# Performance work log

Hardware: AMD Instinct MI355X
Metric: run time of the kernel (lower is better)

The kernel has to match this reference:

```python
import jax, jax.numpy as jnp
import numpy as np

B, S, D, H, F, R = 4, 128, 512, 8, 2048, 8
DH = D // H
THRESH = 0.1  # hardcoded in the torch module


def _ln(x, g, b):
    m = x.mean(-1, keepdims=True)
    v = ((x - m) ** 2).mean(-1, keepdims=True)
    return (x - m) * jax.lax.rsqrt(v + 1e-5) * g + b


def setup_inputs() -> dict:
    key = jax.random.key(0)
    ks = jax.random.split(key, 12)
    w = lambda k, shape, std: jax.random.normal(k, shape, jnp.float32) * std
    s = 1.0 / np.sqrt(D)
    qk_std = 2.0 / np.sqrt(D)  # peaky attention so adjacency threshold fires
    return {
        "x": jax.random.normal(ks[0], (B, S, D), jnp.float32),
        "ln1_g": jnp.ones(D, jnp.float32), "ln1_b": jnp.zeros(D, jnp.float32),
        "wq": w(ks[1], (D, D), qk_std), "bq": jnp.zeros(D, jnp.float32),
        "wk": w(ks[2], (D, D), qk_std), "bk": jnp.zeros(D, jnp.float32),
        "wv": w(ks[3], (D, D), s), "bv": jnp.zeros(D, jnp.float32),
        "wo": w(ks[4], (D, D), s), "bo": jnp.zeros(D, jnp.float32),
        "w1": w(ks[5], (D, F), s), "b1": jnp.zeros(F, jnp.float32),
        "w2": w(ks[6], (F, D), 1.0 / np.sqrt(F)), "b2": jnp.zeros(D, jnp.float32),
        "rc_w1": w(ks[7], (2 * D, D), 1.0 / np.sqrt(2 * D)), "rc_b1": jnp.zeros(D, jnp.float32),
        "rc_w2": w(ks[8], (D, R), s), "rc_b2": jnp.zeros(R, jnp.float32),
        "kg_w": w(ks[9], (R, D, D), s),
        "s2n_w": w(ks[10], (D, D), s), "s2n_b": jnp.zeros(D, jnp.float32),
        "ln2_g": jnp.ones(D, jnp.float32), "ln2_b": jnp.zeros(D, jnp.float32),
    }


def reference(x, ln1_g, ln1_b, wq, bq, wk, bk, wv, bv, wo, bo,
              w1, b1, w2, b2, rc_w1, rc_b1, rc_w2, rc_b2,
              kg_w, s2n_w, s2n_b, ln2_g, ln2_b):
    # pre-norm attention
    xn = _ln(x, ln1_g, ln1_b)
    q = (xn @ wq + bq).reshape(B, S, H, DH)
    k = (xn @ wk + bk).reshape(B, S, H, DH)
    v = (xn @ wv + bv).reshape(B, S, H, DH)
    scores = jnp.einsum('bihd,bjhd->bhij', q, k) / np.sqrt(DH)
    attn = jax.nn.softmax(scores, axis=-1)                  # [B,H,S,S]
    ctx = jnp.einsum('bhij,bjhd->bihd', attn, v).reshape(B, S, D)
    attn_out = ctx @ wo + bo
    # FFN -> neural_understanding (no residual, as in source)
    nu = jax.nn.relu(attn_out @ w1 + b1) @ w2 + b2          # [B,S,D]
    # dynamic edge extraction, expressed as a dense mask (jit-safe)
    am = attn.mean(axis=1)                                  # [B,S,S]
    adj = (am > THRESH) & (~jnp.eye(S, dtype=bool))         # u != v
    # relation classifier on every (u,v) pair; mask selects real edges
    a_part = nu @ rc_w1[:D]                                 # concept1 half
    b_part = nu @ rc_w1[D:]                                 # concept2 half
    h = jax.nn.relu(a_part[:, :, None, :] + b_part[:, None, :, :] + rc_b1)  # [B,S,S,D]
    logits = h @ rc_w2 + rc_b2                              # [B,S,S,R]
    pred = jnp.argmax(logits, axis=-1)
    valid = adj & (pred != 0)                               # relation 0 == NONE
    oh = jax.nn.one_hot(pred, R, dtype=nu.dtype) * valid[..., None].astype(nu.dtype)
    # RGCN-style knowledge graph conv: message u -> v with per-relation weight
    transformed = jnp.einsum('bud,rde->bure', nu, kg_w)     # [B,S,R,D]
    agg = jnp.einsum('buvr,bure->bve', oh, transformed)     # [B,S,D]
    reasoned = nu + agg
    neural_result = reasoned @ s2n_w + s2n_b
    out = _ln(x + neural_result, ln2_g, ln2_b)
    return out
```

## Files before the change

### kernel.cpp

```cpp
#include <hip/hip_runtime.h>
#include <hip/hip_bf16.h>

#define B_ 4
#define S_ 128
#define D_ 512
#define H_ 8
#define DH_ 64
#define F_ 2048
#define R_ 8
#define BS_ (B_ * S_)
#define BSD_ (BS_ * D_)
#define E_ 262144

typedef __attribute__((ext_vector_type(8))) short short8;
typedef __attribute__((ext_vector_type(4))) float f32x4;
typedef __attribute__((ext_vector_type(4))) unsigned short ushort4v;

__device__ __forceinline__ void split2(float a, unsigned short& h, unsigned short& l) {
    unsigned u = __float_as_uint(a);
    unsigned hr = (u + 0x7FFFu + ((u >> 16) & 1u)) >> 16;
    h = (unsigned short)hr;
    float lo = a - __uint_as_float(hr << 16);
    unsigned u2 = __float_as_uint(lo);
    l = (unsigned short)((u2 + 0x7FFFu + ((u2 >> 16) & 1u)) >> 16);
}

struct TDesc { const float* s; unsigned short* h; unsigned short* l; int K; int N; int off; };
struct TPack { TDesc d[10]; };

__global__ void prep_kernel(TPack p, int nt, const float* __restrict__ x,
                            const float* __restrict__ g, const float* __restrict__ be,
                            unsigned short* __restrict__ xh, unsigned short* __restrict__ xl) {
    __shared__ float tr[32][33];
    __shared__ float red[256];
    int bid = blockIdx.x;
    if (bid < nt) {
        int wi = 0;
#pragma unroll
        for (int i = 1; i < 10; ++i) if (bid >= p.d[i].off) wi = i;
        const TDesc dd = p.d[wi];
        int t = bid - dd.off;
        int ntk = dd.K / 32;
        int tk = t % ntk, tn = t / ntk;
        int k0 = tk * 32, n0 = tn * 32;
        int col = threadIdx.x & 31, rg = threadIdx.x >> 5;
#pragma unroll
        for (int i = 0; i < 4; ++i) {
            int row = rg * 4 + i;
            tr[row][col] = dd.s[(size_t)(k0 + row) * dd.N + n0 + col];
        }
        __syncthreads();
#pragma unroll
        for (int i = 0; i < 4; ++i) {
            int n = n0 + rg * 4 + i;
            int k = k0 + col;
            unsigned short h, l;
            split2(tr[col][rg * 4 + i], h, l);
            dd.h[(size_t)n * dd.K + k] = h;
            dd.l[(size_t)n * dd.K + k] = l;
        }
    } else {
        int row = bid - nt;
        int t = threadIdx.x;
        const float* xr = x + (size_t)row * D_;
        float v0 = xr[t], v1 = xr[t + 256];
        red[t] = v0 + v1;
        __syncthreads();
        for (int off = 128; off > 0; off >>= 1) { if (t < off) red[t] += red[t + off]; __syncthreads(); }
        float mean = red[0] * (1.0f / D_);
        __syncthreads();
        float d0 = v0 - mean, d1 = v1 - mean;
        red[t] = d0 * d0 + d1 * d1;
        __syncthreads();
        for (int off = 128; off > 0; off >>= 1) { if (t < off) red[t] += red[t + off]; __syncthreads(); }
        float rs = rsqrtf(red[0] * (1.0f / D_) + 1e-5f);
        float o0 = d0 * rs * g[t] + be[t];
        float o1 = d1 * rs * g[t + 256] + be[t + 256];
        unsigned short h, l;
        split2(o0, h, l); xh[(size_t)row * D_ + t] = h;       xl[(size_t)row * D_ + t] = l;
        split2(o1, h, l); xh[(size_t)row * D_ + t + 256] = h; xl[(size_t)row * D_ + t + 256] = l;
    }
}

struct GemmLds {
    unsigned short A[2][2][64][64];
    unsigned short B[2][2][64][64];
};

__device__ __forceinline__ void gload16(const unsigned short* g, unsigned short* l) {
    __builtin_amdgcn_global_load_lds(
        (const __attribute__((address_space(1))) void*)g,
        (__attribute__((address_space(3))) void*)l, 16, 0, 0);
}

__device__ __forceinline__ void mgemm_core(const unsigned short* __restrict__ Ath,
                                           const unsigned short* __restrict__ Atl,
                                           const unsigned short* __restrict__ Bth,
                                           const unsigned short* __restrict__ Btl,
                                           int K, int rowBase, int colBase,
                                           int kStart, int nsteps,
                                           f32x4 acc[2][2], GemmLds* L) {
    int tid = threadIdx.x;
    int w = tid >> 6, lane = tid & 63;
    int lm = lane & 15, quad = lane >> 4;
    int wm = (w & 1) * 32, wn = (w >> 1) * 32;
    int r0 = w * 8 + (lane >> 3);
    int lc = ((lane & 7) ^ (lane >> 3)) * 8;
    int wb = w * 512;
    size_t a0 = (size_t)(rowBase + r0) * K + kStart + lc;
    size_t a1 = (size_t)(rowBase + r0 + 32) * K + kStart + lc;
    size_t b0 = (size_t)(colBase + r0) * K + kStart + lc;
    size_t b1 = (size_t)(colBase + r0 + 32) * K + kStart + lc;
    unsigned short* AB = &L->A[0][0][0][0];
    unsigned short* BB = &L->B[0][0][0][0];
    auto stage = [&](int p, size_t koff) {
        gload16(&Ath[a0 + koff], AB + p * 8192 + wb);
        gload16(&Ath[a1 + koff], AB + p * 8192 + 2048 + wb);
        gload16(&Atl[a0 + koff], AB + p * 8192 + 4096 + wb);
        gload16(&Atl[a1 + koff], AB + p * 8192 + 6144 + wb);
        gload16(&Bth[b0 + koff], BB + p * 8192 + wb);
        gload16(&Bth[b1 + koff], BB + p * 8192 + 2048 + wb);
        gload16(&Btl[b0 + koff], BB + p * 8192 + 4096 + wb);
        gload16(&Btl[b1 + koff], BB + p * 8192 + 6144 + wb);
    };
    stage(0, 0);
    __syncthreads();
    for (int s = 0; s < nsteps; ++s) {
        int p = s & 1;
        if (s + 1 < nsteps) stage(p ^ 1, (size_t)(s + 1) * 64);
#pragma unroll
        for (int sub = 0; sub < 2; ++sub) {
            short8 ah[2], al[2], bh[2], bl[2];
            int pc = ((sub * 4 + quad) ^ (lm & 7)) * 8;
#pragma unroll
            for (int t = 0; t < 2; ++t) {
                int ra = (wm + t * 16 + lm) * 64 + pc;
                int rb = (wn + t * 16 + lm) * 64 + pc;
                ah[t] = *(const short8*)(AB + p * 8192 + ra);
                al[t] = *(const short8*)(AB + p * 8192 + 4096 + ra);
                bh[t] = *(const short8*)(BB + p * 8192 + rb);
                bl[t] = *(const short8*)(BB + p * 8192 + 4096 + rb);
            }
#pragma unroll
            for (int tm = 0; tm < 2; ++tm)
#pragma unroll
                for (int tn = 0; tn < 2; ++tn) {
                    acc[tm][tn] = __builtin_amdgcn_mfma_f32_16x16x32_bf16(ah[tm], bh[tn], acc[tm][tn], 0, 0, 0);
                    acc[tm][tn] = __builtin_amdgcn_mfma_f32_16x16x32_bf16(ah[tm], bl[tn], acc[tm][tn], 0, 0, 0);
                    acc[tm][tn] = __builtin_amdgcn_mfma_f32_16x16x32_bf16(al[tm], bh[tn], acc[tm][tn], 0, 0, 0);
                }
        }
        __syncthreads();
    }
}

__device__ __forceinline__ void gemm_epilogue(f32x4 acc[2][2], const float* bias,
                                              float* Cf, unsigned short* Ch, unsigned short* Cl,
                                              int N, int relu, int rowBase, int colBase) {
    int tid = threadIdx.x;
    int w = tid >> 6, lane = tid & 63;
    int lm = lane & 15, quad = lane >> 4;
    int wm = (w & 1) * 32, wn = (w >> 1) * 32;
#pragma unroll
    for (int tm = 0; tm < 2; ++tm)
#pragma unroll
        for (int tn = 0; tn < 2; ++tn) {
            int col = colBase + wn + tn * 16 + lm;
            float bi = bias ? bias[col] : 0.f;
#pragma unroll
            for (int r = 0; r < 4; ++r) {
                int row = rowBase + wm + tm * 16 + quad * 4 + r;
                float v = acc[tm][tn][r] + bi;
                if (relu) v = fmaxf(v, 0.f);
                size_t o = (size_t)row * N + col;
                if (Cf) Cf[o] = v;
                if (Ch) {
                    unsigned short sh, sl;
                    split2(v, sh, sl);
                    Ch[o] = sh; Cl[o] = sl;
                }
            }
        }
}

__global__ __launch_bounds__(256) void mgemm_kernel(const unsigned short* __restrict__ Ath,
                                                    const unsigned short* __restrict__ Atl,
                                                    const unsigned short* __restrict__ Bth,
                                                    const unsigned short* __restrict__ Btl,
                                                    const float* __restrict__ bias,
                                                    float* __restrict__ Cf,
                                                    unsigned short* __restrict__ Ch,
                                                    unsigned short* __restrict__ Cl,
                                                    int N, int K, int relu) {
    __shared__ GemmLds L;
    int rowBase = blockIdx.y * 64, colBase = blockIdx.x * 64;
    f32x4 acc[2][2] = {};
    mgemm_core(Ath, Atl, Bth, Btl, K, rowBase, colBase, 0, K / 64, acc, &L);
    gemm_epilogue(acc, bias, Cf, Ch, Cl, N, relu, rowBase, colBase);
}

__global__ __launch_bounds__(256) void mgemm_zw_kernel(const unsigned short* __restrict__ Ath,
                                                       const unsigned short* __restrict__ Atl,
                                                       const unsigned short* __restrict__ Bth,
                                                       const unsigned short* __restrict__ Btl,
                                                       const float* __restrict__ b0,
                                                       const float* __restrict__ b1,
                                                       const float* __restrict__ b2,
                                                       float* __restrict__ Cbase,
                                                       int M, int N, int K) {
    __shared__ GemmLds L;
    int z = blockIdx.z;
    const unsigned short* bth = Bth + (size_t)z * K * N;
    const unsigned short* btl = Btl + (size_t)z * K * N;
    const float* bias = (z == 0) ? b0 : (z == 1) ? b1 : b2;
    float* C = Cbase + (size_t)z * M * N;
    int rowBase = blockIdx.y * 64, colBase = blockIdx.x * 64;
    f32x4 acc[2][2] = {};
    mgemm_core(Ath, Atl, bth, btl, K, rowBase, colBase, 0, K / 64, acc, &L);
    gemm_epilogue(acc, bias, C, nullptr, nullptr, N, 0, rowBase, colBase);
}

__global__ __launch_bounds__(256) void mgemm_part_kernel(const unsigned short* __restrict__ Ath,
                                                         const unsigned short* __restrict__ Atl,
                                                         const unsigned short* __restrict__ Bth,
                                                         const unsigned short* __restrict__ Btl,
                                                         float* __restrict__ Cbase,
                                                         int M, int N, int K) {
    __shared__ GemmLds L;
    int ks = gridDim.z, z = blockIdx.z;
    int kLen = K / ks, kStart = z * kLen;
    float* C = Cbase + (size_t)z * M * N;
    int rowBase = blockIdx.y * 64, colBase = blockIdx.x * 64;
    f32x4 acc[2][2] = {};
    mgemm_core(Ath, Atl, Bth, Btl, K, rowBase, colBase, kStart, kLen / 64, acc, &L);
    gemm_epilogue(acc, nullptr, C, nullptr, nullptr, N, 0, rowBase, colBase);
}

__global__ __launch_bounds__(256) void wo_adj_kernel(const unsigned short* __restrict__ Ath,
                                                     const unsigned short* __restrict__ Atl,
                                                     const unsigned short* __restrict__ Bth,
                                                     const unsigned short* __restrict__ Btl,
                                                     const float* __restrict__ bias,
                                                     unsigned short* __restrict__ Ch,
                                                     unsigned short* __restrict__ Cl,
                                                     const float* __restrict__ attnP,
                                                     unsigned long long* __restrict__ adjm) {
    __shared__ GemmLds L;
    int bid = blockIdx.x;
    if (bid < 64) {
        int rowBase = (bid >> 3) * 64, colBase = (bid & 7) * 64;
        f32x4 acc[2][2] = {};
        mgemm_core(Ath, Atl, Bth, Btl, D_, rowBase, colBase, 0, D_ / 64, acc, &L);
        gemm_epilogue(acc, bias, nullptr, Ch, Cl, D_, 0, rowBase, colBase);
    } else {
        int idx = (bid - 64) * 256 + threadIdx.x;
        int j = idx & (S_ - 1);
        int bi = idx >> 7;
        int i = bi & (S_ - 1);
        int b = bi >> 7;
        float s = 0.f;
#pragma unroll
        for (int h = 0; h < H_; ++h) s += attnP[(((size_t)(b * H_ + h)) * S_ + i) * S_ + j];
        s *= (1.0f / H_);
        int pred = (s > 0.1f && i != j) ? 1 : 0;
        unsigned long long m = __ballot(pred);
        if ((threadIdx.x & 63) == 0)
            adjm[(size_t)bi * 2 + ((threadIdx.x >> 6) & 1)] = m;
    }
}

__global__ void reduce4_kernel(const float* __restrict__ part, const float* __restrict__ b2,
                               float* __restrict__ nu,
                               unsigned short* __restrict__ nh, unsigned short* __restrict__ nl) {
    int base = blockIdx.x * 1024 + threadIdx.x * 4;
    f32x4 s = *(const f32x4*)&b2[base & (D_ - 1)];
#pragma unroll
    for (int z = 0; z < 4; ++z) s += *(const f32x4*)&part[(size_t)z * BSD_ + base];
    *(f32x4*)&nu[base] = s;
    ushort4v hv, lv;
#pragma unroll
    for (int i = 0; i < 4; ++i) { unsigned short h, l; split2(s[i], h, l); hv[i] = h; lv[i] = l; }
    *(ushort4v*)&nh[base] = hv;
    *(ushort4v*)&nl[base] = lv;
}

__global__ void reduce8_kernel(const float* __restrict__ part, const float* __restrict__ nu,
                               unsigned short* __restrict__ rh, unsigned short* __restrict__ rl) {
    int base = blockIdx.x * 1024 + threadIdx.x * 4;
    f32x4 s = *(const f32x4*)&nu[base];
#pragma unroll
    for (int z = 0; z < 8; ++z) s += *(const f32x4*)&part[(size_t)z * BSD_ + base];
    ushort4v hv, lv;
#pragma unroll
    for (int i = 0; i < 4; ++i) { unsigned short h, l; split2(s[i], h, l); hv[i] = h; lv[i] = l; }
    *(ushort4v*)&rh[base] = hv;
    *(ushort4v*)&rl[base] = lv;
}

__global__ __launch_bounds__(512) void attn_kernel2(const float* __restrict__ q,
                                                    const float* __restrict__ k,
                                                    const float* __restrict__ v,
                                                    float* __restrict__ attnP,
                                                    unsigned short* __restrict__ ch,
                                                    unsigned short* __restrict__ cl) {
    __shared__ float ksm[S_][DH_ + 3];
    __shared__ float qsm[16][DH_];
    __shared__ float psm[16][S_];
    int tid = threadIdx.x;
    int w = tid >> 6, lane = tid & 63;
    int blk = blockIdx.x;
    int ig = blk & 7;
    int bh = blk >> 3;
    int h = bh & (H_ - 1);
    int b = bh >> 3;
    int i0 = ig * 16;
    const float* kb = k + (size_t)b * S_ * D_ + h * DH_;
    for (int j = w; j < S_; j += 8) ksm[j][lane] = kb[(size_t)j * D_ + lane];
    for (int il = w; il < 16; il += 8)
        qsm[il][lane] = q[(size_t)(b * S_ + i0 + il) * D_ + h * DH_ + lane];
    __syncthreads();
    const float* vb = v + (size_t)b * S_ * D_ + h * DH_ + lane;
#pragma unroll
    for (int c = 0; c < 2; ++c) {
        int il = w + c * 8;
        int i = i0 + il;
        float s0 = 0.f, s1 = 0.f;
#pragma unroll 8
        for (int d = 0; d < DH_; ++d) {
            float qd = qsm[il][d];
            s0 += qd * ksm[lane][d];
            s1 += qd * ksm[lane + 64][d];
        }
        s0 *= 0.125f; s1 *= 0.125f;
        float m = fmaxf(s0, s1);
#pragma unroll
        for (int off = 32; off > 0; off >>= 1) m = fmaxf(m, __shfl_xor(m, off));
        float e0 = __expf(s0 - m), e1 = __expf(s1 - m);
        float sum = e0 + e1;
#pragma unroll
        for (int off = 32; off > 0; off >>= 1) sum += __shfl_xor(sum, off);
        float inv = 1.f / sum;
        float p0 = e0 * inv, p1 = e1 * inv;
        float* arow = attnP + ((size_t)(b * H_ + h) * S_ + i) * S_;
        arow[lane] = p0;
        arow[lane + 64] = p1;
        psm[il][lane] = p0;
        psm[il][lane + 64] = p1;
        float acc = 0.f;
        for (int j = 0; j < S_; ++j) acc += psm[il][j] * vb[(size_t)j * D_];
        unsigned short sh, sl;
        split2(acc, sh, sl);
        size_t o = (size_t)(b * S_ + i) * D_ + h * DH_ + lane;
        ch[o] = sh; cl[o] = sl;
    }
}

__global__ __launch_bounds__(512) void mbuild_edge_kernel(const float* __restrict__ nu,
                                                          const float* __restrict__ a_part,
                                                          const float* __restrict__ b_part,
                                                          const float* __restrict__ rc_b1,
                                                          const float* __restrict__ rc_w2,
                                                          const float* __restrict__ rc_b2,
                                                          const unsigned long long* __restrict__ adjm,
                                                          unsigned short* __restrict__ Mh,
                                                          unsigned short* __restrict__ Ml) {
    __shared__ float acc[R_ * D_];
    __shared__ float w2t[R_][D_];
    __shared__ float bsm[D_];
    __shared__ int rl[S_];
    int blk = blockIdx.x;
    int vv = blk & (S_ - 1);
    int b = blk >> 7;
    int t = threadIdx.x;
    int w = t >> 6, lane = t & 63;
    for (int i = t; i < R_ * D_; i += 512) {
        w2t[i & 7][i >> 3] = rc_w2[i];
        acc[i] = 0.f;
    }
    bsm[t] = b_part[(size_t)blk * D_ + t];
    __syncthreads();
    int wsel = vv >> 6, bsh = vv & 63;
    for (int u = w; u < S_; u += 8) {
        unsigned long long word = adjm[((size_t)(b * S_ + u)) * 2 + wsel];
        if ((word >> bsh) & 1ull) {
            const float* ap = a_part + (size_t)(b * S_ + u) * D_;
            float lp[R_];
#pragma unroll
            for (int r = 0; r < R_; ++r) lp[r] = 0.f;
#pragma unroll
            for (int jj = 0; jj < D_ / 64; ++jj) {
                int d = lane + jj * 64;
                float hv = fmaxf(ap[d] + bsm[d] + rc_b1[d], 0.f);
#pragma unroll
                for (int r = 0; r < R_; ++r) lp[r] += hv * w2t[r][d];
            }
#pragma unroll
            for (int r = 0; r < R_; ++r) {
#pragma unroll
                for (int off = 32; off > 0; off >>= 1) lp[r] += __shfl_down(lp[r], off);
            }
            if (lane == 0) {
                float best = lp[0] + rc_b2[0];
                int bi = 0;
#pragma unroll
                for (int r = 1; r < R_; ++r) {
                    float L = lp[r] + rc_b2[r];
                    if (L > best) { best = L; bi = r; }
                }
                rl[u] = bi;
            }
        } else if (lane == 0) {
            rl[u] = 0;
        }
    }
    __syncthreads();
    for (int u = 0; u < S_; ++u) {
        int r = rl[u];
        if (r > 0) acc[r * D_ + t] += nu[(size_t)(b * S_ + u) * D_ + t];
    }
    __syncthreads();
    unsigned short* Hrow = Mh + (size_t)blk * (R_ * D_);
    unsigned short* Lrow = Ml + (size_t)blk * (R_ * D_);
    for (int i = t; i < R_ * D_; i += 512) {
        unsigned short sh, sl;
        split2(acc[i], sh, sl);
        Hrow[i] = sh; Lrow[i] = sl;
    }
}

__global__ void ln2_kernel(const float* __restrict__ x, const float* __restrict__ y,
                           const float* __restrict__ g, const float* __restrict__ be,
                           float* __restrict__ out) {
    int row = blockIdx.x;
    int t = threadIdx.x;
    __shared__ float red[256];
    float v0 = x[row * D_ + t]       + y[row * D_ + t];
    float v1 = x[row * D_ + t + 256] + y[row * D_ + t + 256];
    red[t] = v0 + v1;
    __syncthreads();
    for (int off = 128; off > 0; off >>= 1) {
        if (t < off) red[t] += red[t + off];
        __syncthreads();
    }
    float mean = red[0] * (1.0f / D_);
    __syncthreads();
    float d0 = v0 - mean, d1 = v1 - mean;
    red[t] = d0 * d0 + d1 * d1;
    __syncthreads();
    for (int off = 128; off > 0; off >>= 1) {
        if (t < off) red[t] += red[t + off];
        __syncthreads();
    }
    float rs = rsqrtf(red[0] * (1.0f / D_) + 1e-5f);
    out[row * D_ + t]       = d0 * rs * g[t]       + be[t];
    out[row * D_ + t + 256] = d1 * rs * g[t + 256] + be[t + 256];
}

extern "C" void kernel_launch(void* const* d_in, const int* in_sizes, int n_in,
                              void* d_out, int out_size, void* d_ws, size_t ws_size,
                              hipStream_t stream) {
    const float* x     = (const float*)d_in[0];
    const float* ln1_g = (const float*)d_in[1];
    const float* ln1_b = (const float*)d_in[2];
    const float* wq    = (const float*)d_in[3];
    const float* bq    = (const float*)d_in[4];
    const float* wk    = (const float*)d_in[5];
    const float* bk    = (const float*)d_in[6];
    const float* wv    = (const float*)d_in[7];
    const float* bv    = (const float*)d_in[8];
    const float* wo    = (const float*)d_in[9];
    const float* bo    = (const float*)d_in[10];
    const float* w1    = (const float*)d_in[11];
    const float* b1    = (const float*)d_in[12];
    const float* w2    = (const float*)d_in[13];
    const float* b2    = (const float*)d_in[14];
    const float* rc_w1 = (const float*)d_in[15];
    const float* rc_b1 = (const float*)d_in[16];
    const float* rc_w2 = (const float*)d_in[17];
    const float* rc_b2 = (const float*)d_in[18];
    const float* kg_w  = (const float*)d_in[19];
    const float* s2n_w = (const float*)d_in[20];
    const float* s2n_b = (const float*)d_in[21];
    const float* ln2_g = (const float*)d_in[22];
    const float* ln2_b = (const float*)d_in[23];
    float* out = (float*)d_out;

    const int BS  = BS_;
    const int BSD = BSD_;

    unsigned short* wt = (unsigned short*)d_ws;
    unsigned short* qkv_h = wt;
    unsigned short* qkv_l = wt + 3 * E_;
    unsigned short* wo_h  = wt + 6 * E_;
    unsigned short* wo_l  = wt + 7 * E_;
    unsigned short* w1_h  = wt + 8 * E_;
    unsigned short* w1_l  = wt + 12 * E_;
    unsigned short* w2_h  = wt + 16 * E_;
    unsigned short* w2_l  = wt + 20 * E_;
    unsigned short* rc_h  = wt + 24 * E_;
    unsigned short* rc_l  = wt + 26 * E_;
    unsigned short* kg_h  = wt + 28 * E_;
    unsigned short* kg_l  = wt + 36 * E_;
    unsigned short* s2_h  = wt + 44 * E_;
    unsigned short* s2_l  = wt + 45 * E_;

    unsigned short* xn_h  = wt + 46 * E_;
    unsigned short* xn_l  = xn_h + BSD;
    unsigned short* ctx_h = xn_l + BSD;
    unsigned short* ctx_l = ctx_h + BSD;
    unsigned short* ao_h  = ctx_l + BSD;
    unsigned short* ao_l  = ao_h + BSD;
    unsigned short* hid_h = ao_l + BSD;
    unsigned short* hid_l = hid_h + (size_t)BS * F_;
    unsigned short* nu_h  = hid_l + (size_t)BS * F_;
    unsigned short* nu_l  = nu_h + BSD;
    unsigned short* mb_h  = nu_l + BSD;
    unsigned short* mb_l  = mb_h + (size_t)BS * R_ * D_;
    unsigned short* rs_h  = mb_l + (size_t)BS * R_ * D_;
    unsigned short* rs_l  = rs_h + BSD;

    float* fbase  = (float*)(rs_l + BSD);
    float* q      = fbase;
    float* v_     = q + 2 * BSD;
    float* apart  = q + 3 * BSD;
    float* nu     = apart + 2 * BSD;
    float* y      = nu + BSD;
    float* part4  = y + BSD;
    float* part8  = part4 + 4 * BSD;
    float* attnP  = part8 + 8 * BSD;

    unsigned long long* adjm = (unsigned long long*)(attnP + 2097152);

    TPack tp;
    int off = 0;
    auto setd = [&](int i, const float* s, unsigned short* h, unsigned short* l, int K, int N) {
        tp.d[i] = TDesc{s, h, l, K, N, off};
        off += (K / 32) * (N / 32);
    };
    setd(0, wq, qkv_h,          qkv_l,          D_, D_);
    setd(1, wk, qkv_h + E_,     qkv_l + E_,     D_, D_);
    setd(2, wv, qkv_h + 2 * E_, qkv_l + 2 * E_, D_, D_);
    setd(3, wo, wo_h, wo_l, D_, D_);
    setd(4, w1, w1_h, w1_l, D_, F_);
    setd(5, w2, w2_h, w2_l, F_, D_);
    setd(6, rc_w1,            rc_h,      rc_l,      D_, D_);
    setd(7, rc_w1 + D_ * D_,  rc_h + E_, rc_l + E_, D_, D_);
    setd(8, kg_w, kg_h, kg_l, R_ * D_, D_);
    setd(9, s2n_w, s2_h, s2_l, D_, D_);
    hipLaunchKernelGGL(prep_kernel, dim3(off + BS), dim3(256), 0, stream, tp, off,
                       x, ln1_g, ln1_b, xn_h, xn_l);

    hipLaunchKernelGGL(mgemm_zw_kernel, dim3(D_ / 64, BS / 64, 3), dim3(256), 0, stream,
                       xn_h, xn_l, qkv_h, qkv_l, bq, bk, bv, q, BS, D_, D_);
    hipLaunchKernelGGL(attn_kernel2, dim3(B_ * H_ * 8), dim3(512), 0, stream,
                       q, q + BSD, v_, attnP, ctx_h, ctx_l);
    hipLaunchKernelGGL(wo_adj_kernel, dim3(64 + 256), dim3(256), 0, stream,
                       ctx_h, ctx_l, wo_h, wo_l, bo, ao_h, ao_l, attnP, adjm);
    hipLaunchKernelGGL(mgemm_kernel, dim3(F_ / 64, BS / 64), dim3(256), 0, stream,
                       ao_h, ao_l, w1_h, w1_l, b1, (float*)nullptr, hid_h, hid_l, F_, D_, 1);
    hipLaunchKernelGGL(mgemm_part_kernel, dim3(D_ / 64, BS / 64, 4), dim3(256), 0, stream,
                       hid_h, hid_l, w2_h, w2_l, part4, BS, D_, F_);
    hipLaunchKernelGGL(reduce4_kernel, dim3(BSD / 1024), dim3(256), 0, stream,
                       part4, b2, nu, nu_h, nu_l);
    hipLaunchKernelGGL(mgemm_zw_kernel, dim3(D_ / 64, BS / 64, 2), dim3(256), 0, stream,
                       nu_h, nu_l, rc_h, rc_l, (const float*)nullptr, (const float*)nullptr,
                       (const float*)nullptr, apart, BS, D_, D_);
    hipLaunchKernelGGL(mbuild_edge_kernel, dim3(BS), dim3(512), 0, stream,
                       nu, apart, apart + BSD, rc_b1, rc_w2, rc_b2, adjm, mb_h, mb_l);
    hipLaunchKernelGGL(mgemm_part_kernel, dim3(D_ / 64, BS / 64, 8), dim3(256), 0, stream,
                       mb_h, mb_l, kg_h, kg_l, part8, BS, D_, R_ * D_);
    hipLaunchKernelGGL(reduce8_kernel, dim3(BSD / 1024), dim3(256), 0, stream,
                       part8, nu, rs_h, rs_l);
    hipLaunchKernelGGL(mgemm_kernel, dim3(D_ / 64, BS / 64), dim3(256), 0, stream,
                       rs_h, rs_l, s2_h, s2_l, s2n_b, y, (unsigned short*)nullptr,
                       (unsigned short*)nullptr, D_, D_, 0);
    hipLaunchKernelGGL(ln2_kernel, dim3(BS), dim3(256), 0, stream, x, y, ln2_g, ln2_b, out);
}
```

Measured before the change: 224.1 us.

## Triple-buffer GEMM LDS staging with explicit vmcnt waits

Moves the split-bf16 GEMM core from double to triple buffering in LDS, keeping up to two future K-steps of global-to-LDS loads in flight. Plain __syncthreads is replaced by explicit s_waitcnt vmcnt counts plus s_barrier and sched_barrier, so each step waits only for its own batch of loads. This should hide more global latency, but LDS use grows by half, which may cut occupancy. The hand-counted vmcnt values also rely on no other outstanding vector memory ops.

```diff
diff --git a/kernel.cpp b/kernel.cpp
--- a/kernel.cpp
+++ b/kernel.cpp
@@ -83,14 +83,20 @@
 }
 
 struct GemmLds {
-    unsigned short A[2][2][64][64];
-    unsigned short B[2][2][64][64];
+    unsigned short A[3][2][64][64];
+    unsigned short B[3][2][64][64];
 };
 
 __device__ __forceinline__ void gload16(const unsigned short* g, unsigned short* l) {
     __builtin_amdgcn_global_load_lds(
         (const __attribute__((address_space(1))) void*)g,
         (__attribute__((address_space(3))) void*)l, 16, 0, 0);
+}
+
+__device__ __forceinline__ void vmwait_batches(int nb) {
+    if (nb == 2)      asm volatile("s_waitcnt vmcnt(16)" ::: "memory");
+    else if (nb == 1) asm volatile("s_waitcnt vmcnt(8)" ::: "memory");
+    else              asm volatile("s_waitcnt vmcnt(0)" ::: "memory");
 }
 
 __device__ __forceinline__ void mgemm_core(const unsigned short* __restrict__ Ath,
@@ -113,21 +119,26 @@
     size_t b1 = (size_t)(colBase + r0 + 32) * K + kStart + lc;
     unsigned short* AB = &L->A[0][0][0][0];
     unsigned short* BB = &L->B[0][0][0][0];
-    auto stage = [&](int p, size_t koff) {
-        gload16(&Ath[a0 + koff], AB + p * 8192 + wb);
-        gload16(&Ath[a1 + koff], AB + p * 8192 + 2048 + wb);
-        gload16(&Atl[a0 + koff], AB + p * 8192 + 4096 + wb);
-        gload16(&Atl[a1 + koff], AB + p * 8192 + 6144 + wb);
-        gload16(&Bth[b0 + koff], BB + p * 8192 + wb);
-        gload16(&Bth[b1 + koff], BB + p * 8192 + 2048 + wb);
-        gload16(&Btl[b0 + koff], BB + p * 8192 + 4096 + wb);
-        gload16(&Btl[b1 + koff], BB + p * 8192 + 6144 + wb);
+    auto stage = [&](int buf, size_t koff) {
+        gload16(&Ath[a0 + koff], AB + buf * 8192 + wb);
+        gload16(&Ath[a1 + koff], AB + buf * 8192 + 2048 + wb);
+        gload16(&Atl[a0 + koff], AB + buf * 8192 + 4096 + wb);
+        gload16(&Atl[a1 + koff], AB + buf * 8192 + 6144 + wb);
+        gload16(&Bth[b0 + koff], BB + buf * 8192 + wb);
+        gload16(&Bth[b1 + koff], BB + buf * 8192 + 2048 + wb);
+        gload16(&Btl[b0 + koff], BB + buf * 8192 + 4096 + wb);
+        gload16(&Btl[b1 + koff], BB + buf * 8192 + 6144 + wb);
     };
     stage(0, 0);
-    __syncthreads();
+    if (nsteps > 1) stage(1, 64);
+    if (nsteps > 2) stage(2, 128);
+    int b = 0;
     for (int s = 0; s < nsteps; ++s) {
-        int p = s & 1;
-        if (s + 1 < nsteps) stage(p ^ 1, (size_t)(s + 1) * 64);
+        int last = nsteps - 1;
+        int inflight = (s + 2 <= last) ? 2 : (s + 1 <= last) ? 1 : 0;
+        vmwait_batches(inflight);
+        __builtin_amdgcn_s_barrier();
+        __builtin_amdgcn_sched_barrier(0);
 #pragma unroll
         for (int sub = 0; sub < 2; ++sub) {
             short8 ah[2], al[2], bh[2], bl[2];
@@ -136,10 +147,10 @@
             for (int t = 0; t < 2; ++t) {
                 int ra = (wm + t * 16 + lm) * 64 + pc;
                 int rb = (wn + t * 16 + lm) * 64 + pc;
-                ah[t] = *(const short8*)(AB + p * 8192 + ra);
-                al[t] = *(const short8*)(AB + p * 8192 + 4096 + ra);
-                bh[t] = *(const short8*)(BB + p * 8192 + rb);
-                bl[t] = *(const short8*)(BB + p * 8192 + 4096 + rb);
+                ah[t] = *(const short8*)(AB + b * 8192 + ra);
+                al[t] = *(const short8*)(AB + b * 8192 + 4096 + ra);
+                bh[t] = *(const short8*)(BB + b * 8192 + rb);
+                bl[t] = *(const short8*)(BB + b * 8192 + 4096 + rb);
             }
 #pragma unroll
             for (int tm = 0; tm < 2; ++tm)
@@ -150,7 +161,10 @@
                     acc[tm][tn] = __builtin_amdgcn_mfma_f32_16x16x32_bf16(al[tm], bh[tn], acc[tm][tn], 0, 0, 0);
                 }
         }
-        __syncthreads();
+        __builtin_amdgcn_sched_barrier(0);
+        __builtin_amdgcn_s_barrier();
+        if (s + 3 < nsteps) stage(b, (size_t)(s + 3) * 64);
+        b = (b == 2) ? 0 : b + 1;
     }
 }
 
```

Result: no change. 220.1 us (-1.8%).
